# Kernel tuning notes

Measured on AMD Instinct MI355X. Metric: run time of the kernel, lower is better.

The kernel has to match this reference:

```python
import jax, jax.numpy as jnp
import numpy as np

N_NODES = 100000
N_EDGES = 3200000
IN_C, HID_C, OUT_C = 5, 128, 64


def setup_inputs() -> dict:
    key = jax.random.key(0)
    k_x, k_e, k_w1, k_b1, k_w2, k_b2 = jax.random.split(key, 6)
    x = jax.random.normal(k_x, (N_NODES, IN_C), dtype=jnp.float32)
    edge_index = jax.random.randint(k_e, (2, N_EDGES), 0, N_NODES, dtype=jnp.int32)
    # GCNConv learned params (glorot weights, zero-ish bias)
    W1 = jax.random.normal(k_w1, (IN_C, HID_C), dtype=jnp.float32) * (1.0 / np.sqrt(IN_C))
    b1 = jax.random.normal(k_b1, (HID_C,), dtype=jnp.float32) * 0.01
    W2 = jax.random.normal(k_w2, (HID_C, OUT_C), dtype=jnp.float32) * (1.0 / np.sqrt(HID_C))
    b2 = jax.random.normal(k_b2, (OUT_C,), dtype=jnp.float32) * 0.01
    return {"x": x, "edge_index": edge_index, "W1": W1, "b1": b1, "W2": W2, "b2": b2}


def _gcn_conv(x, src, dst, deg_inv_sqrt, W, b):
    """One GCNConv (PyG defaults: self-loops already in src/dst, symmetric norm, bias)."""
    h = x @ W                                   # [N, C_out]
    norm = deg_inv_sqrt[src] * deg_inv_sqrt[dst]  # [E+N]
    msg = h[src] * norm[:, None]                # gather + scale
    out = jax.ops.segment_sum(msg, dst, num_segments=x.shape[0])  # scatter-add
    return out + b


def reference(x, edge_index, W1, b1, W2, b2):
    n = x.shape[0]
    loop = jnp.arange(n, dtype=edge_index.dtype)
    src = jnp.concatenate([edge_index[0], loop])  # self-loops appended
    dst = jnp.concatenate([edge_index[1], loop])
    deg = jax.ops.segment_sum(jnp.ones_like(src, dtype=x.dtype), dst, num_segments=n)
    deg_inv_sqrt = jnp.where(deg > 0, jax.lax.rsqrt(deg), 0.0)
    h = _gcn_conv(x, src, dst, deg_inv_sqrt, W1, b1)
    z = _gcn_conv(h, src, dst, deg_inv_sqrt, W2, b2)
    return z
```

## Files before the change

kernel.cpp:

```cpp
#include <hip/hip_runtime.h>

#define IN_C  5
#define HID_C 128
#define OUT_C 64

#define KB   256
#define NBP  512
#define CAP  10240
#define TILE 4096
#define BTH  512
#define EPT  (TILE / BTH)
#define EPTV (TILE / BTH / 4)
#define GNODES 64

typedef int      vi4 __attribute__((ext_vector_type(4)));
typedef float    vf4 __attribute__((ext_vector_type(4)));
typedef _Float16 vh8 __attribute__((ext_vector_type(8)));


__global__ __launch_bounds__(BTH) void k_bin(const int* __restrict__ src,
                                             const int* __restrict__ dstp,
                                             int* __restrict__ gcursor,
                                             int* __restrict__ binned, int e) {
    __shared__ int lhist[NBP];
    __shared__ int lgofs[NBP];
    __shared__ int lbeg[NBP];
    __shared__ int lsort[TILE];
    __shared__ int gdst[TILE];
    __shared__ int wsum[8];
    __shared__ int stot;
    int tid = threadIdx.x;
    int lane = tid & 63, w = tid >> 6;
    int tbeg = blockIdx.x * TILE;
    lhist[tid] = 0;
    __syncthreads();
    int pk[EPT], bk[EPT], rk[EPT];
    #pragma unroll
    for (int q = 0; q < EPTV; ++q) {
        int idx = tbeg + (q * BTH + tid) * 4;
        if (idx < e) {
            vi4 s4 = __builtin_nontemporal_load((const vi4*)(src + idx));
            vi4 d4 = __builtin_nontemporal_load((const vi4*)(dstp + idx));
            pk[q*4+0] = ((d4.x & 255) << 24) | s4.x; bk[q*4+0] = ((unsigned)d4.x) >> 8;
            pk[q*4+1] = ((d4.y & 255) << 24) | s4.y; bk[q*4+1] = ((unsigned)d4.y) >> 8;
            pk[q*4+2] = ((d4.z & 255) << 24) | s4.z; bk[q*4+2] = ((unsigned)d4.z) >> 8;
            pk[q*4+3] = ((d4.w & 255) << 24) | s4.w; bk[q*4+3] = ((unsigned)d4.w) >> 8;
            rk[q*4+0] = atomicAdd(&lhist[bk[q*4+0]], 1);
            rk[q*4+1] = atomicAdd(&lhist[bk[q*4+1]], 1);
            rk[q*4+2] = atomicAdd(&lhist[bk[q*4+2]], 1);
            rk[q*4+3] = atomicAdd(&lhist[bk[q*4+3]], 1);
        } else {
            bk[q*4+0] = -1; bk[q*4+1] = -1; bk[q*4+2] = -1; bk[q*4+3] = -1;
        }
    }
    __syncthreads();
    int h = lhist[tid];
    int v = h;
    #pragma unroll
    for (int m = 1; m < 64; m <<= 1) { int u = __shfl_up(v, m); if (lane >= m) v += u; }
    if (lane == 63) wsum[w] = v;
    __syncthreads();
    if (tid == 0) {
        int s = 0;
        #pragma unroll
        for (int k = 0; k < 8; ++k) { int tv = wsum[k]; wsum[k] = s; s += tv; }
    }
    __syncthreads();
    int excl = wsum[w] + v - h;
    lbeg[tid] = excl;
    if (h > 0)
        lgofs[tid] = tid * CAP + atomicAdd(&gcursor[tid], h) - excl;
    if (tid == BTH - 1) stot = excl + h;
    __syncthreads();
    #pragma unroll
    for (int q = 0; q < EPT; ++q) {
        if (bk[q] >= 0) {
            int slot = lbeg[bk[q]] + rk[q];
            lsort[slot] = pk[q];
            gdst[slot] = lgofs[bk[q]] + slot;
        }
    }
    __syncthreads();
    int tot = stot;
    for (int i = tid; i < tot; i += BTH)
        binned[gdst[i]] = lsort[i];
}

__global__ __launch_bounds__(BTH) void k_build(int* __restrict__ binned,
                                               const int* __restrict__ gcursor,
                                               const float* __restrict__ x,
                                               int2* __restrict__ pse,
                                               _Float16* __restrict__ xs, int n) {
    __shared__ int cnt[KB];
    __shared__ int wt[4];
    __shared__ int wte[4];
    __shared__ int stage[CAP];
    int tid = threadIdx.x;
    int lane = tid & 63, w = tid >> 6;
    int bkt = blockIdx.x;
    int beg = bkt * CAP;
    int tot = gcursor[bkt];
    if (tid < KB) cnt[tid] = 0;
    __syncthreads();
    int4 r[5];
    int4 rr[5];
    #pragma unroll
    for (int it = 0; it < 5; ++it) {
        int j0 = (tid << 2) + it * (BTH * 4);
        if (j0 < tot) {
            r[it] = *(const int4*)(binned + beg + j0);
            rr[it].x = atomicAdd(&cnt[((unsigned)r[it].x) >> 24], 1);
            if (j0 + 1 < tot) rr[it].y = atomicAdd(&cnt[((unsigned)r[it].y) >> 24], 1);
            if (j0 + 2 < tot) rr[it].z = atomicAdd(&cnt[((unsigned)r[it].z) >> 24], 1);
            if (j0 + 3 < tot) rr[it].w = atomicAdd(&cnt[((unsigned)r[it].w) >> 24], 1);
        }
    }
    __syncthreads();
    int deg = (tid < KB) ? cnt[tid] : 0;
    int v = deg;
    #pragma unroll
    for (int m = 1; m < 64; m <<= 1) { int u = __shfl_up(v, m); if (lane >= m) v += u; }
    if (tid < KB && lane == 63) wt[w] = v;
    __syncthreads();
    if (tid == 0) {
        int s = 0;
        #pragma unroll
        for (int k = 0; k < 4; ++k) { wte[k] = s; s += wt[k]; }
    }
    __syncthreads();
    if (tid < KB) {
        int rel = wte[w] + v - deg;
        int node = bkt * KB + tid;
        pse[node] = make_int2(beg + rel, beg + rel + deg);
        cnt[tid] = rel;
        float d = rsqrtf(1.0f + (float)deg);
        vh8 hq = {};
        if (node < n) {
            hq[0] = (_Float16)(x[node * IN_C + 0] * d);
            hq[1] = (_Float16)(x[node * IN_C + 1] * d);
            hq[2] = (_Float16)(x[node * IN_C + 2] * d);
            hq[3] = (_Float16)(x[node * IN_C + 3] * d);
            hq[4] = (_Float16)(x[node * IN_C + 4] * d);
            hq[5] = (_Float16)d;
        }
        *((vh8*)(xs + (size_t)node * 8)) = hq;
    }
    __syncthreads();
    #pragma unroll
    for (int it = 0; it < 5; ++it) {
        int j0 = (tid << 2) + it * (BTH * 4);
        if (j0 < tot) {
            stage[cnt[((unsigned)r[it].x) >> 24] + rr[it].x] = r[it].x & 0xFFFFFF;
            if (j0 + 1 < tot)
                stage[cnt[((unsigned)r[it].y) >> 24] + rr[it].y] = r[it].y & 0xFFFFFF;
            if (j0 + 2 < tot)
                stage[cnt[((unsigned)r[it].z) >> 24] + rr[it].z] = r[it].z & 0xFFFFFF;
            if (j0 + 3 < tot)
                stage[cnt[((unsigned)r[it].w) >> 24] + rr[it].w] = r[it].w & 0xFFFFFF;
        }
    }
    __syncthreads();
    for (int j = tid; j < tot; j += BTH)
        binned[beg + j] = stage[j];
}

__global__ __launch_bounds__(BTH) void k_gath0(const int* __restrict__ srclist,
                                               const int2* __restrict__ pse,
                                               const _Float16* __restrict__ feat,
                                               _Float16* __restrict__ outf,
                                               float* __restrict__ tout, int n) {
    int tid = threadIdx.x;
    int node = blockIdx.x * GNODES + (tid >> 3);
    int sub = tid & 7;
    if (node >= n) return;
    int2 pp = pse[node];
    int ps = pp.x, pe = pp.y;
    float a0 = 0, a1 = 0, a2 = 0, a3 = 0, a4 = 0, a5 = 0;
    int j = ps + sub;
    for (; j + 24 < pe; j += 32) {
        int s0 = srclist[j],      s1 = srclist[j + 8];
        int s2 = srclist[j + 16], s3 = srclist[j + 24];
        vh8 h0 = *(const vh8*)(feat + (size_t)s0 * 8);
        vh8 h1 = *(const vh8*)(feat + (size_t)s1 * 8);
        vh8 h2 = *(const vh8*)(feat + (size_t)s2 * 8);
        vh8 h3 = *(const vh8*)(feat + (size_t)s3 * 8);
        a0 += ((float)h0[0] + (float)h1[0]) + ((float)h2[0] + (float)h3[0]);
        a1 += ((float)h0[1] + (float)h1[1]) + ((float)h2[1] + (float)h3[1]);
        a2 += ((float)h0[2] + (float)h1[2]) + ((float)h2[2] + (float)h3[2]);
        a3 += ((float)h0[3] + (float)h1[3]) + ((float)h2[3] + (float)h3[3]);
        a4 += ((float)h0[4] + (float)h1[4]) + ((float)h2[4] + (float)h3[4]);
        a5 += ((float)h0[5] + (float)h1[5]) + ((float)h2[5] + (float)h3[5]);
    }
    for (; j < pe; j += 8) {
        int sA = srclist[j];
        vh8 hA = *(const vh8*)(feat + (size_t)sA * 8);
        a0 += (float)hA[0]; a1 += (float)hA[1]; a2 += (float)hA[2];
        a3 += (float)hA[3]; a4 += (float)hA[4]; a5 += (float)hA[5];
    }
    #pragma unroll
    for (int m = 1; m < 8; m <<= 1) {
        a0 += __shfl_xor(a0, m);
        a1 += __shfl_xor(a1, m);
        a2 += __shfl_xor(a2, m);
        a3 += __shfl_xor(a3, m);
        a4 += __shfl_xor(a4, m);
        a5 += __shfl_xor(a5, m);
    }
    if (sub == 0) {
        vh8 hs = *(const vh8*)(feat + (size_t)node * 8);
        float d = (float)hs[5];
        a0 += (float)hs[0]; a1 += (float)hs[1]; a2 += (float)hs[2];
        a3 += (float)hs[3]; a4 += (float)hs[4]; a5 += d;
        float d2 = d * d;
        vh8 ho = {};
        ho[0] = (_Float16)(d2 * a0);
        ho[1] = (_Float16)(d2 * a1);
        ho[2] = (_Float16)(d2 * a2);
        ho[3] = (_Float16)(d2 * a3);
        ho[4] = (_Float16)(d2 * a4);
        ho[5] = (_Float16)d;
        tout[node] = d * a5;
        *((vh8*)(outf + (size_t)node * 8)) = ho;
    }
}

__global__ __launch_bounds__(BTH) void k_gout(const int* __restrict__ srclist,
                                              const int2* __restrict__ pse,
                                              const _Float16* __restrict__ feat,
                                              const float* __restrict__ t,
                                              const float* __restrict__ W1,
                                              const float* __restrict__ b1,
                                              const float* __restrict__ W2,
                                              const float* __restrict__ b2,
                                              float* __restrict__ out, int n) {
    __shared__ float snode[GNODES * 8];
    __shared__ float sW[IN_C * OUT_C + 2 * OUT_C];
    int tid = threadIdx.x;
    if (tid < IN_C * OUT_C) {
        int k = tid >> 6, c = tid & 63;
        float acc = 0.0f;
        for (int m = 0; m < HID_C; ++m)
            acc += W1[k * HID_C + m] * W2[m * OUT_C + c];
        sW[tid] = acc;
    } else if (tid < IN_C * OUT_C + OUT_C) {
        int c = tid - IN_C * OUT_C;
        float acc = 0.0f;
        for (int m = 0; m < HID_C; ++m)
            acc += b1[m] * W2[m * OUT_C + c];
        sW[tid] = acc;
    } else if (tid < IN_C * OUT_C + 2 * OUT_C) {
        sW[tid] = b2[tid - IN_C * OUT_C - OUT_C];
    }
    int node = blockIdx.x * GNODES + (tid >> 3);
    int sub = tid & 7;
    bool act = (node < n);
    float a0 = 0, a1 = 0, a2 = 0, a3 = 0, a4 = 0;
    if (act) {
        int2 pp = pse[node];
        int ps = pp.x, pe = pp.y;
        int j = ps + sub;
        for (; j + 24 < pe; j += 32) {
            int s0 = srclist[j],      s1 = srclist[j + 8];
            int s2 = srclist[j + 16], s3 = srclist[j + 24];
            vh8 h0 = *(const vh8*)(feat + (size_t)s0 * 8);
            vh8 h1 = *(const vh8*)(feat + (size_t)s1 * 8);
            vh8 h2 = *(const vh8*)(feat + (size_t)s2 * 8);
            vh8 h3 = *(const vh8*)(feat + (size_t)s3 * 8);
            a0 += ((float)h0[0] + (float)h1[0]) + ((float)h2[0] + (float)h3[0]);
            a1 += ((float)h0[1] + (float)h1[1]) + ((float)h2[1] + (float)h3[1]);
            a2 += ((float)h0[2] + (float)h1[2]) + ((float)h2[2] + (float)h3[2]);
            a3 += ((float)h0[3] + (float)h1[3]) + ((float)h2[3] + (float)h3[3]);
            a4 += ((float)h0[4] + (float)h1[4]) + ((float)h2[4] + (float)h3[4]);
        }
        for (; j < pe; j += 8) {
            int sA = srclist[j];
            vh8 hA = *(const vh8*)(feat + (size_t)sA * 8);
            a0 += (float)hA[0]; a1 += (float)hA[1]; a2 += (float)hA[2];
            a3 += (float)hA[3]; a4 += (float)hA[4];
        }
    }
    #pragma unroll
    for (int m = 1; m < 8; m <<= 1) {
        a0 += __shfl_xor(a0, m);
        a1 += __shfl_xor(a1, m);
        a2 += __shfl_xor(a2, m);
        a3 += __shfl_xor(a3, m);
        a4 += __shfl_xor(a4, m);
    }
    if (act && sub == 0) {
        vh8 hs = *(const vh8*)(feat + (size_t)node * 8);
        float d = (float)hs[5];
        a0 += (float)hs[0]; a1 += (float)hs[1]; a2 += (float)hs[2];
        a3 += (float)hs[3]; a4 += (float)hs[4];
        float* sn = snode + (tid >> 3) * 8;
        sn[0] = d * a0; sn[1] = d * a1; sn[2] = d * a2;
        sn[3] = d * a3; sn[4] = d * a4; sn[5] = t[node];
    }
    __syncthreads();
    int base = blockIdx.x * GNODES;
    for (int u = tid; u < GNODES * 16; u += BTH) {
        int ln = u >> 4, q = u & 15;
        int i = base + ln;
        if (i >= n) continue;
        const float* a = snode + ln * 8;
        float ti = a[5];
        float4 acc = ((const float4*)(sW + IN_C * OUT_C + OUT_C))[q];
        float4 bq  = ((const float4*)(sW + IN_C * OUT_C))[q];
        acc.x += ti * bq.x; acc.y += ti * bq.y;
        acc.z += ti * bq.z; acc.w += ti * bq.w;
        #pragma unroll
        for (int k = 0; k < IN_C; ++k) {
            float ak = a[k];
            float4 wk = ((const float4*)(sW + k * OUT_C))[q];
            acc.x += ak * wk.x; acc.y += ak * wk.y;
            acc.z += ak * wk.z; acc.w += ak * wk.w;
        }
        vf4 av; av.x = acc.x; av.y = acc.y; av.z = acc.z; av.w = acc.w;
        __builtin_nontemporal_store(av, ((vf4*)out) + (size_t)i * 16 + q);
    }
}

extern "C" void kernel_launch(void* const* d_in, const int* in_sizes, int n_in,
                              void* d_out, int out_size, void* d_ws, size_t ws_size,
                              hipStream_t stream) {
    const float* x   = (const float*)d_in[0];
    const int*   ei  = (const int*)d_in[1];
    const float* W1  = (const float*)d_in[2];
    const float* b1  = (const float*)d_in[3];
    const float* W2  = (const float*)d_in[4];
    const float* b2  = (const float*)d_in[5];
    float* out = (float*)d_out;

    const int n = in_sizes[0] / IN_C;
    const int e = in_sizes[1] / 2;
    const int* src = ei;
    const int* dst = ei + e;
    const int NB = (n + KB - 1) / KB;
    const int NKB = NB * KB;

    int*      gcursor = (int*)d_ws;
    int*      binned  = gcursor + 512;
    int2*     pse     = (int2*)(binned + (size_t)NBP * CAP);
    _Float16* xs      = (_Float16*)(pse + NKB);
    _Float16* p1      = xs + (size_t)8 * NKB;
    float*    t       = (float*)(p1 + (size_t)8 * NKB);

    const int gB = (e + TILE - 1) / TILE;
    const int gG = (n + GNODES - 1) / GNODES;

    (void)hipMemsetAsync(gcursor, 0, NBP * sizeof(int), stream);
    k_bin   <<<gB, BTH, 0, stream>>>(src, dst, gcursor, binned, e);
    k_build <<<NB, BTH, 0, stream>>>(binned, gcursor, x, pse, xs, n);
    k_gath0 <<<gG, BTH, 0, stream>>>(binned, pse, xs, p1, t, n);
    k_gout  <<<gG, BTH, 0, stream>>>(binned, pse, p1, t,
                                     W1, b1, W2, b2, out, n);
}
```

Measured before the change: 173.0 us.

## Fuse bucket sort into gather kernels with per-node degree atomics

Degree counting moves into the binning kernel as global atomics, so a simple prep kernel can build the normalized fp16 features without a per-bucket sort pass. Each gather kernel now reads its own bucket of 128 destinations, re-sorts it locally in shared memory and gathers straight from the staged source list. This removes the separate build pass, the CSR offset array and the t array, which now rides in an unused fp16 lane. The cost is 3.2M global atomics on random addresses, the sort done twice (once per layer), hard-coded bucket counts tied to N, and t stored in fp16.

```diff
diff --git a/kernel.cpp b/kernel.cpp
--- a/kernel.cpp
+++ b/kernel.cpp
@@ -4,14 +4,14 @@
 #define HID_C 128
 #define OUT_C 64
 
-#define KB   256
-#define NBP  512
-#define CAP  10240
+#define KB   128
+#define NBP  1024
+#define NBR  782
+#define CAP  5120
 #define TILE 4096
 #define BTH  512
 #define EPT  (TILE / BTH)
 #define EPTV (TILE / BTH / 4)
-#define GNODES 64
 
 typedef int      vi4 __attribute__((ext_vector_type(4)));
 typedef float    vf4 __attribute__((ext_vector_type(4)));
@@ -21,6 +21,7 @@
 __global__ __launch_bounds__(BTH) void k_bin(const int* __restrict__ src,
                                              const int* __restrict__ dstp,
                                              int* __restrict__ gcursor,
+                                             int* __restrict__ deg,
                                              int* __restrict__ binned, int e) {
     __shared__ int lhist[NBP];
     __shared__ int lgofs[NBP];
@@ -32,7 +33,7 @@
     int tid = threadIdx.x;
     int lane = tid & 63, w = tid >> 6;
     int tbeg = blockIdx.x * TILE;
-    lhist[tid] = 0;
+    lhist[tid] = 0; lhist[tid + BTH] = 0;
     __syncthreads();
     int pk[EPT], bk[EPT], rk[EPT];
     #pragma unroll
@@ -41,21 +42,26 @@
         if (idx < e) {
             vi4 s4 = __builtin_nontemporal_load((const vi4*)(src + idx));
             vi4 d4 = __builtin_nontemporal_load((const vi4*)(dstp + idx));
-            pk[q*4+0] = ((d4.x & 255) << 24) | s4.x; bk[q*4+0] = ((unsigned)d4.x) >> 8;
-            pk[q*4+1] = ((d4.y & 255) << 24) | s4.y; bk[q*4+1] = ((unsigned)d4.y) >> 8;
-            pk[q*4+2] = ((d4.z & 255) << 24) | s4.z; bk[q*4+2] = ((unsigned)d4.z) >> 8;
-            pk[q*4+3] = ((d4.w & 255) << 24) | s4.w; bk[q*4+3] = ((unsigned)d4.w) >> 8;
+            pk[q*4+0] = ((d4.x & 127) << 24) | s4.x; bk[q*4+0] = ((unsigned)d4.x) >> 7;
+            pk[q*4+1] = ((d4.y & 127) << 24) | s4.y; bk[q*4+1] = ((unsigned)d4.y) >> 7;
+            pk[q*4+2] = ((d4.z & 127) << 24) | s4.z; bk[q*4+2] = ((unsigned)d4.z) >> 7;
+            pk[q*4+3] = ((d4.w & 127) << 24) | s4.w; bk[q*4+3] = ((unsigned)d4.w) >> 7;
             rk[q*4+0] = atomicAdd(&lhist[bk[q*4+0]], 1);
             rk[q*4+1] = atomicAdd(&lhist[bk[q*4+1]], 1);
             rk[q*4+2] = atomicAdd(&lhist[bk[q*4+2]], 1);
             rk[q*4+3] = atomicAdd(&lhist[bk[q*4+3]], 1);
+            atomicAdd(&deg[d4.x], 1);
+            atomicAdd(&deg[d4.y], 1);
+            atomicAdd(&deg[d4.z], 1);
+            atomicAdd(&deg[d4.w], 1);
         } else {
             bk[q*4+0] = -1; bk[q*4+1] = -1; bk[q*4+2] = -1; bk[q*4+3] = -1;
         }
     }
     __syncthreads();
-    int h = lhist[tid];
-    int v = h;
+    int hA = lhist[2 * tid], hB = lhist[2 * tid + 1];
+    int hp = hA + hB;
+    int v = hp;
     #pragma unroll
     for (int m = 1; m < 64; m <<= 1) { int u = __shfl_up(v, m); if (lane >= m) v += u; }
     if (lane == 63) wsum[w] = v;
@@ -66,11 +72,15 @@
         for (int k = 0; k < 8; ++k) { int tv = wsum[k]; wsum[k] = s; s += tv; }
     }
     __syncthreads();
-    int excl = wsum[w] + v - h;
-    lbeg[tid] = excl;
-    if (h > 0)
-        lgofs[tid] = tid * CAP + atomicAdd(&gcursor[tid], h) - excl;
-    if (tid == BTH - 1) stot = excl + h;
+    int exclP = wsum[w] + v - hp;
+    lbeg[2 * tid] = exclP;
+    lbeg[2 * tid + 1] = exclP + hA;
+    if (hA > 0)
+        lgofs[2 * tid] = (2 * tid) * CAP + atomicAdd(&gcursor[2 * tid], hA) - exclP;
+    if (hB > 0)
+        lgofs[2 * tid + 1] = (2 * tid + 1) * CAP +
+                             atomicAdd(&gcursor[2 * tid + 1], hB) - (exclP + hA);
+    if (tid == BTH - 1) stot = exclP + hp;
     __syncthreads();
     #pragma unroll
     for (int q = 0; q < EPT; ++q) {
@@ -86,100 +96,82 @@
         binned[gdst[i]] = lsort[i];
 }
 
-__global__ __launch_bounds__(BTH) void k_build(int* __restrict__ binned,
-                                               const int* __restrict__ gcursor,
-                                               const float* __restrict__ x,
-                                               int2* __restrict__ pse,
-                                               _Float16* __restrict__ xs, int n) {
-    __shared__ int cnt[KB];
-    __shared__ int wt[4];
-    __shared__ int wte[4];
+__global__ __launch_bounds__(BTH) void k_prep(const float* __restrict__ x,
+                                              const int* __restrict__ deg,
+                                              _Float16* __restrict__ xs, int n) {
+    int node = blockIdx.x * BTH + threadIdx.x;
+    if (node >= NBR * KB) return;
+    vh8 hq = {};
+    if (node < n) {
+        float d = rsqrtf(1.0f + (float)deg[node]);
+        hq[0] = (_Float16)(x[node * IN_C + 0] * d);
+        hq[1] = (_Float16)(x[node * IN_C + 1] * d);
+        hq[2] = (_Float16)(x[node * IN_C + 2] * d);
+        hq[3] = (_Float16)(x[node * IN_C + 3] * d);
+        hq[4] = (_Float16)(x[node * IN_C + 4] * d);
+        hq[5] = (_Float16)d;
+    }
+    *((vh8*)(xs + (size_t)node * 8)) = hq;
+}
+
+__global__ __launch_bounds__(BTH) void k_g1(const int* __restrict__ binned,
+                                            const int* __restrict__ gcursor,
+                                            const _Float16* __restrict__ feat,
+                                            _Float16* __restrict__ outf, int n) {
+    __shared__ int dcnt[KB];
+    __shared__ int seg[KB];
     __shared__ int stage[CAP];
+    __shared__ int wt[2];
     int tid = threadIdx.x;
     int lane = tid & 63, w = tid >> 6;
     int bkt = blockIdx.x;
     int beg = bkt * CAP;
     int tot = gcursor[bkt];
-    if (tid < KB) cnt[tid] = 0;
-    __syncthreads();
-    int4 r[5];
-    int4 rr[5];
-    #pragma unroll
-    for (int it = 0; it < 5; ++it) {
+    if (tid < KB) dcnt[tid] = 0;
+    __syncthreads();
+    int4 r[3], rr[3];
+    #pragma unroll
+    for (int it = 0; it < 3; ++it) {
         int j0 = (tid << 2) + it * (BTH * 4);
         if (j0 < tot) {
             r[it] = *(const int4*)(binned + beg + j0);
-            rr[it].x = atomicAdd(&cnt[((unsigned)r[it].x) >> 24], 1);
-            if (j0 + 1 < tot) rr[it].y = atomicAdd(&cnt[((unsigned)r[it].y) >> 24], 1);
-            if (j0 + 2 < tot) rr[it].z = atomicAdd(&cnt[((unsigned)r[it].z) >> 24], 1);
-            if (j0 + 3 < tot) rr[it].w = atomicAdd(&cnt[((unsigned)r[it].w) >> 24], 1);
-        }
-    }
-    __syncthreads();
-    int deg = (tid < KB) ? cnt[tid] : 0;
-    int v = deg;
+            rr[it].x = atomicAdd(&dcnt[((unsigned)r[it].x) >> 24], 1);
+            if (j0 + 1 < tot) rr[it].y = atomicAdd(&dcnt[((unsigned)r[it].y) >> 24], 1);
+            if (j0 + 2 < tot) rr[it].z = atomicAdd(&dcnt[((unsigned)r[it].z) >> 24], 1);
+            if (j0 + 3 < tot) rr[it].w = atomicAdd(&dcnt[((unsigned)r[it].w) >> 24], 1);
+        }
+    }
+    __syncthreads();
+    int dg = (tid < KB) ? dcnt[tid] : 0;
+    int v = dg;
     #pragma unroll
     for (int m = 1; m < 64; m <<= 1) { int u = __shfl_up(v, m); if (lane >= m) v += u; }
     if (tid < KB && lane == 63) wt[w] = v;
     __syncthreads();
-    if (tid == 0) {
-        int s = 0;
-        #pragma unroll
-        for (int k = 0; k < 4; ++k) { wte[k] = s; s += wt[k]; }
-    }
-    __syncthreads();
-    if (tid < KB) {
-        int rel = wte[w] + v - deg;
-        int node = bkt * KB + tid;
-        pse[node] = make_int2(beg + rel, beg + rel + deg);
-        cnt[tid] = rel;
-        float d = rsqrtf(1.0f + (float)deg);
-        vh8 hq = {};
-        if (node < n) {
-            hq[0] = (_Float16)(x[node * IN_C + 0] * d);
-            hq[1] = (_Float16)(x[node * IN_C + 1] * d);
-            hq[2] = (_Float16)(x[node * IN_C + 2] * d);
-            hq[3] = (_Float16)(x[node * IN_C + 3] * d);
-            hq[4] = (_Float16)(x[node * IN_C + 4] * d);
-            hq[5] = (_Float16)d;
-        }
-        *((vh8*)(xs + (size_t)node * 8)) = hq;
-    }
-    __syncthreads();
-    #pragma unroll
-    for (int it = 0; it < 5; ++it) {
+    if (tid < KB) seg[tid] = (w == 1 ? wt[0] : 0) + v - dg;
+    __syncthreads();
+    #pragma unroll
+    for (int it = 0; it < 3; ++it) {
         int j0 = (tid << 2) + it * (BTH * 4);
         if (j0 < tot) {
-            stage[cnt[((unsigned)r[it].x) >> 24] + rr[it].x] = r[it].x & 0xFFFFFF;
+            stage[seg[((unsigned)r[it].x) >> 24] + rr[it].x] = r[it].x & 0xFFFFFF;
             if (j0 + 1 < tot)
-                stage[cnt[((unsigned)r[it].y) >> 24] + rr[it].y] = r[it].y & 0xFFFFFF;
+                stage[seg[((unsigned)r[it].y) >> 24] + rr[it].y] = r[it].y & 0xFFFFFF;
             if (j0 + 2 < tot)
-                stage[cnt[((unsigned)r[it].z) >> 24] + rr[it].z] = r[it].z & 0xFFFFFF;
+                stage[seg[((unsigned)r[it].z) >> 24] + rr[it].z] = r[it].z & 0xFFFFFF;
             if (j0 + 3 < tot)
-                stage[cnt[((unsigned)r[it].w) >> 24] + rr[it].w] = r[it].w & 0xFFFFFF;
-        }
-    }
-    __syncthreads();
-    for (int j = tid; j < tot; j += BTH)
-        binned[beg + j] = stage[j];
-}
-
-__global__ __launch_bounds__(BTH) void k_gath0(const int* __restrict__ srclist,
-                                               const int2* __restrict__ pse,
-                                               const _Float16* __restrict__ feat,
-                                               _Float16* __restrict__ outf,
-                                               float* __restrict__ tout, int n) {
-    int tid = threadIdx.x;
-    int node = blockIdx.x * GNODES + (tid >> 3);
-    int sub = tid & 7;
+                stage[seg[((unsigned)r[it].w) >> 24] + rr[it].w] = r[it].w & 0xFFFFFF;
+        }
+    }
+    __syncthreads();
+    int nd = tid >> 2, sub = tid & 3;
+    int node = bkt * KB + nd;
     if (node >= n) return;
-    int2 pp = pse[node];
-    int ps = pp.x, pe = pp.y;
+    int ps = seg[nd], pe = ps + dcnt[nd];
     float a0 = 0, a1 = 0, a2 = 0, a3 = 0, a4 = 0, a5 = 0;
     int j = ps + sub;
-    for (; j + 24 < pe; j += 32) {
-        int s0 = srclist[j],      s1 = srclist[j + 8];
-        int s2 = srclist[j + 16], s3 = srclist[j + 24];
+    for (; j + 12 < pe; j += 16) {
+        int s0 = stage[j], s1 = stage[j + 4], s2 = stage[j + 8], s3 = stage[j + 12];
         vh8 h0 = *(const vh8*)(feat + (size_t)s0 * 8);
         vh8 h1 = *(const vh8*)(feat + (size_t)s1 * 8);
         vh8 h2 = *(const vh8*)(feat + (size_t)s2 * 8);
@@ -191,14 +183,14 @@
         a4 += ((float)h0[4] + (float)h1[4]) + ((float)h2[4] + (float)h3[4]);
         a5 += ((float)h0[5] + (float)h1[5]) + ((float)h2[5] + (float)h3[5]);
     }
-    for (; j < pe; j += 8) {
-        int sA = srclist[j];
+    for (; j < pe; j += 4) {
+        int sA = stage[j];
         vh8 hA = *(const vh8*)(feat + (size_t)sA * 8);
         a0 += (float)hA[0]; a1 += (float)hA[1]; a2 += (float)hA[2];
         a3 += (float)hA[3]; a4 += (float)hA[4]; a5 += (float)hA[5];
     }
     #pragma unroll
-    for (int m = 1; m < 8; m <<= 1) {
+    for (int m = 1; m < 4; m <<= 1) {
         a0 += __shfl_xor(a0, m);
         a1 += __shfl_xor(a1, m);
         a2 += __shfl_xor(a2, m);
@@ -219,23 +211,27 @@
         ho[3] = (_Float16)(d2 * a3);
         ho[4] = (_Float16)(d2 * a4);
         ho[5] = (_Float16)d;
-        tout[node] = d * a5;
+        ho[6] = (_Float16)(d * a5);
         *((vh8*)(outf + (size_t)node * 8)) = ho;
     }
 }
 
-__global__ __launch_bounds__(BTH) void k_gout(const int* __restrict__ srclist,
-                                              const int2* __restrict__ pse,
-                                              const _Float16* __restrict__ feat,
-                                              const float* __restrict__ t,
-                                              const float* __restrict__ W1,
-                                              const float* __restrict__ b1,
-                                              const float* __restrict__ W2,
-                                              const float* __restrict__ b2,
-                                              float* __restrict__ out, int n) {
-    __shared__ float snode[GNODES * 8];
+__global__ __launch_bounds__(BTH) void k_g2(const int* __restrict__ binned,
+                                            const int* __restrict__ gcursor,
+                                            const _Float16* __restrict__ feat,
+                                            const float* __restrict__ W1,
+                                            const float* __restrict__ b1,
+                                            const float* __restrict__ W2,
+                                            const float* __restrict__ b2,
+                                            float* __restrict__ out, int n) {
+    __shared__ int dcnt[KB];
+    __shared__ int seg[KB];
+    __shared__ int stage[CAP];
+    __shared__ int wt[2];
+    __shared__ float snode[KB * 8];
     __shared__ float sW[IN_C * OUT_C + 2 * OUT_C];
     int tid = threadIdx.x;
+    int lane = tid & 63, w = tid >> 6;
     if (tid < IN_C * OUT_C) {
         int k = tid >> 6, c = tid & 63;
         float acc = 0.0f;
@@ -251,17 +247,55 @@
     } else if (tid < IN_C * OUT_C + 2 * OUT_C) {
         sW[tid] = b2[tid - IN_C * OUT_C - OUT_C];
     }
-    int node = blockIdx.x * GNODES + (tid >> 3);
-    int sub = tid & 7;
+    int bkt = blockIdx.x;
+    int beg = bkt * CAP;
+    int tot = gcursor[bkt];
+    if (tid < KB) dcnt[tid] = 0;
+    __syncthreads();
+    int4 r[3], rr[3];
+    #pragma unroll
+    for (int it = 0; it < 3; ++it) {
+        int j0 = (tid << 2) + it * (BTH * 4);
+        if (j0 < tot) {
+            r[it] = *(const int4*)(binned + beg + j0);
+            rr[it].x = atomicAdd(&dcnt[((unsigned)r[it].x) >> 24], 1);
+            if (j0 + 1 < tot) rr[it].y = atomicAdd(&dcnt[((unsigned)r[it].y) >> 24], 1);
+            if (j0 + 2 < tot) rr[it].z = atomicAdd(&dcnt[((unsigned)r[it].z) >> 24], 1);
+            if (j0 + 3 < tot) rr[it].w = atomicAdd(&dcnt[((unsigned)r[it].w) >> 24], 1);
+        }
+    }
+    __syncthreads();
+    int dg = (tid < KB) ? dcnt[tid] : 0;
+    int v = dg;
+    #pragma unroll
+    for (int m = 1; m < 64; m <<= 1) { int u = __shfl_up(v, m); if (lane >= m) v += u; }
+    if (tid < KB && lane == 63) wt[w] = v;
+    __syncthreads();
+    if (tid < KB) seg[tid] = (w == 1 ? wt[0] : 0) + v - dg;
+    __syncthreads();
+    #pragma unroll
+    for (int it = 0; it < 3; ++it) {
+        int j0 = (tid << 2) + it * (BTH * 4);
+        if (j0 < tot) {
+            stage[seg[((unsigned)r[it].x) >> 24] + rr[it].x] = r[it].x & 0xFFFFFF;
+            if (j0 + 1 < tot)
+                stage[seg[((unsigned)r[it].y) >> 24] + rr[it].y] = r[it].y & 0xFFFFFF;
+            if (j0 + 2 < tot)
+                stage[seg[((unsigned)r[it].z) >> 24] + rr[it].z] = r[it].z & 0xFFFFFF;
+            if (j0 + 3 < tot)
+                stage[seg[((unsigned)r[it].w) >> 24] + rr[it].w] = r[it].w & 0xFFFFFF;
+        }
+    }
+    __syncthreads();
+    int nd = tid >> 2, sub = tid & 3;
+    int node = bkt * KB + nd;
     bool act = (node < n);
     float a0 = 0, a1 = 0, a2 = 0, a3 = 0, a4 = 0;
     if (act) {
-        int2 pp = pse[node];
-        int ps = pp.x, pe = pp.y;
+        int ps = seg[nd], pe = ps + dcnt[nd];
         int j = ps + sub;
-        for (; j + 24 < pe; j += 32) {
-            int s0 = srclist[j],      s1 = srclist[j + 8];
-            int s2 = srclist[j + 16], s3 = srclist[j + 24];
+        for (; j + 12 < pe; j += 16) {
+            int s0 = stage[j], s1 = stage[j + 4], s2 = stage[j + 8], s3 = stage[j + 12];
             vh8 h0 = *(const vh8*)(feat + (size_t)s0 * 8);
             vh8 h1 = *(const vh8*)(feat + (size_t)s1 * 8);
             vh8 h2 = *(const vh8*)(feat + (size_t)s2 * 8);
@@ -272,15 +306,15 @@
             a3 += ((float)h0[3] + (float)h1[3]) + ((float)h2[3] + (float)h3[3]);
             a4 += ((float)h0[4] + (float)h1[4]) + ((float)h2[4] + (float)h3[4]);
         }
-        for (; j < pe; j += 8) {
-            int sA = srclist[j];
+        for (; j < pe; j += 4) {
+            int sA = stage[j];
             vh8 hA = *(const vh8*)(feat + (size_t)sA * 8);
             a0 += (float)hA[0]; a1 += (float)hA[1]; a2 += (float)hA[2];
             a3 += (float)hA[3]; a4 += (float)hA[4];
         }
     }
     #pragma unroll
-    for (int m = 1; m < 8; m <<= 1) {
+    for (int m = 1; m < 4; m <<= 1) {
         a0 += __shfl_xor(a0, m);
         a1 += __shfl_xor(a1, m);
         a2 += __shfl_xor(a2, m);
@@ -292,13 +326,13 @@
         float d = (float)hs[5];
         a0 += (float)hs[0]; a1 += (float)hs[1]; a2 += (float)hs[2];
         a3 += (float)hs[3]; a4 += (float)hs[4];
-        float* sn = snode + (tid >> 3) * 8;
+        float* sn = snode + nd * 8;
         sn[0] = d * a0; sn[1] = d * a1; sn[2] = d * a2;
-        sn[3] = d * a3; sn[4] = d * a4; sn[5] = t[node];
-    }
-    __syncthreads();
-    int base = blockIdx.x * GNODES;
-    for (int u = tid; u < GNODES * 16; u += BTH) {
+        sn[3] = d * a3; sn[4] = d * a4; sn[5] = (float)hs[6];
+    }
+    __syncthreads();
+    int base = bkt * KB;
+    for (int u = tid; u < KB * 16; u += BTH) {
         int ln = u >> 4, q = u & 15;
         int i = base + ln;
         if (i >= n) continue;
@@ -335,23 +369,21 @@
     const int e = in_sizes[1] / 2;
     const int* src = ei;
     const int* dst = ei + e;
-    const int NB = (n + KB - 1) / KB;
-    const int NKB = NB * KB;
+    const int NKB = NBR * KB;
 
     int*      gcursor = (int*)d_ws;
-    int*      binned  = gcursor + 512;
-    int2*     pse     = (int2*)(binned + (size_t)NBP * CAP);
-    _Float16* xs      = (_Float16*)(pse + NKB);
+    int*      deg     = gcursor + NBP;
+    int*      binned  = deg + NKB;
+    _Float16* xs      = (_Float16*)(binned + (size_t)NBP * CAP);
     _Float16* p1      = xs + (size_t)8 * NKB;
-    float*    t       = (float*)(p1 + (size_t)8 * NKB);
 
     const int gB = (e + TILE - 1) / TILE;
-    const int gG = (n + GNODES - 1) / GNODES;
-
-    (void)hipMemsetAsync(gcursor, 0, NBP * sizeof(int), stream);
-    k_bin   <<<gB, BTH, 0, stream>>>(src, dst, gcursor, binned, e);
-    k_build <<<NB, BTH, 0, stream>>>(binned, gcursor, x, pse, xs, n);
-    k_gath0 <<<gG, BTH, 0, stream>>>(binned, pse, xs, p1, t, n);
-    k_gout  <<<gG, BTH, 0, stream>>>(binned, pse, p1, t,
+    const int gP = (NKB + BTH - 1) / BTH;
+
+    (void)hipMemsetAsync(gcursor, 0, (NBP + NKB) * sizeof(int), stream);
+    k_bin  <<<gB,  BTH, 0, stream>>>(src, dst, gcursor, deg, binned, e);
+    k_prep <<<gP,  BTH, 0, stream>>>(x, deg, xs, n);
+    k_g1   <<<NBR, BTH, 0, stream>>>(binned, gcursor, xs, p1, n);
+    k_g2   <<<NBR, BTH, 0, stream>>>(binned, gcursor, p1,
                                      W1, b1, W2, b2, out, n);
 }
```

Measured after the change: 296.5 us. 71.4% more time.
